# Kernel tuning notes

Measured on AMD Instinct MI355X. Metric: run time of the kernel, lower is better.

Reference implementation:

```python
import jax, jax.numpy as jnp
import numpy as np

# --- SLAYER hyperparameters (from netParams) ---
THETA = 10.0        # spike threshold
TAU_SR = 10.0       # SRM alpha-kernel time constant (ms)
TAU_RHO = 1.0       # surrogate-gradient width
SCALE_RHO = 1.0     # surrogate-gradient scale
TS = 1.0            # simulation step (ms)
T_SAMPLE = 300      # number of time steps
K_LEN = 64          # truncated SRM kernel length

N_BATCH, N_IN, N_HID, N_OUT = 128, 784, 410, 10


def srm_kernel():
    # SRM-alpha kernel eps(t) = (t/tau) * exp(1 - t/tau), sampled at Ts, eps(0)=0
    t = jnp.arange(K_LEN, dtype=jnp.float32) * TS
    return (t / TAU_SR) * jnp.exp(1.0 - t / TAU_SR)


def psp(x):
    # Causal FIR filtering along time: out[t] = sum_k eps[k] * x[t-k]
    # x: [N, C, T]
    n, c, t = x.shape
    kern = srm_kernel()
    lhs = x.reshape(n * c, 1, t)
    rhs = kern[::-1].reshape(1, 1, K_LEN)  # flip: conv_general_dilated is cross-correlation
    out = jax.lax.conv_general_dilated(
        lhs, rhs, window_strides=(1,), padding=[(K_LEN - 1, 0)],
        dimension_numbers=("NCH", "OIH", "NCH"))
    return out.reshape(n, c, t)


@jax.custom_vjp
def spike_fn(u):
    # Heaviside threshold with surrogate gradient rho(u) = (scale/tau) * exp(-|u-theta|/tau)
    return (u >= THETA).astype(u.dtype)

def _spike_fwd(u):
    return spike_fn(u), u

def _spike_bwd(u, g):
    return (g * (SCALE_RHO / TAU_RHO) * jnp.exp(-jnp.abs(u - THETA) / TAU_RHO),)

spike_fn.defvjp(_spike_fwd, _spike_bwd)


def setup_inputs() -> dict:
    key = jax.random.key(0)
    k1, k2, k3, k4 = jax.random.split(key, 4)
    img = jax.random.uniform(k1, (N_BATCH, N_IN), dtype=jnp.float32)
    rand_u = jax.random.uniform(k2, (N_BATCH, N_IN, T_SAMPLE), dtype=jnp.float32)
    W1 = jax.random.normal(k3, (N_HID, N_IN), dtype=jnp.float32)
    W2 = jax.random.normal(k4, (N_OUT, N_HID), dtype=jnp.float32)
    return {"img": img, "rand_u": rand_u, "W1": W1, "W2": W2}


def reference(img, rand_u, W1, W2):
    # Poisson spike encoding: spike whenever uniform noise < pixel intensity
    s0 = (rand_u < img[:, :, None]).astype(jnp.float32)        # [N, 784, T]
    # fc1 (dense over spatial features, shared over time) -> psp -> spike
    a1 = jnp.einsum("nit,oi->not", s0, W1)                     # [N, 410, T]
    s1 = spike_fn(psp(a1))
    # fc2 -> psp -> spike
    a2 = jnp.einsum("nht,oh->not", s1, W2)                     # [N, 10, T]
    s2 = spike_fn(psp(a2))
    return s2
```

## Files before the change

### kernel.cpp

```cpp
#include <hip/hip_runtime.h>
#include <cstdint>
#include <cstddef>

#define N_B 128
#define N_I 784
#define N_H 410
#define N_O 10
#define TT  300
#define KL  64
#define NK  832
#define NKS 13
#define NTILES 26
#define NDIG 4
#define NKS2 7
#define S1_TILE 4800
#define S1_NSTRIDE 134400
#define SEGL 19
#define SEGL2 10
#define NWG1 (NTILES * N_B)
#define WPX  (NWG1 / 8)
#define DBYTES (NTILES * NKS * 1024)

typedef int v4i __attribute__((ext_vector_type(4)));

__device__ __forceinline__ void glds16(const void* g, void* l) {
  __builtin_amdgcn_global_load_lds(
      (const __attribute__((address_space(1))) uint32_t*)g,
      (__attribute__((address_space(3))) uint32_t*)l, 16, 0, 0);
}

__global__ void k_pack(const float* __restrict__ rand_u, const float* __restrict__ img,
                       uint8_t* __restrict__ s0b) {
  int t = blockIdx.x * 64 + threadIdx.x;
  int w2 = blockIdx.y;
  int n = blockIdx.z;
  if (t >= TT) return;
  const float* rb = rand_u + (size_t)n * N_I * TT + t;
  const float* ib = img + (size_t)n * N_I;
  uint8_t* dst = s0b + ((size_t)n * TT + t) * NK + w2 * 64;
  int kb = w2 * 64;
  #pragma unroll
  for (int g = 0; g < 4; ++g) {
    uint32_t wd[4];
    #pragma unroll
    for (int q = 0; q < 4; ++q) {
      uint32_t v = 0;
      #pragma unroll
      for (int b = 0; b < 4; ++b) {
        int i = kb + g * 16 + q * 4 + b;
        float r = (i < N_I) ? rb[(size_t)i * TT] : 2.0f;
        float p = (i < N_I) ? ib[i] : 0.0f;
        v |= (r < p ? 1u : 0u) << (8 * b);
      }
      wd[q] = v;
    }
    v4i o; o[0] = (int)wd[0]; o[1] = (int)wd[1]; o[2] = (int)wd[2]; o[3] = (int)wd[3];
    *(v4i*)(dst + g * 16) = o;
  }
}

__global__ void k_bprepall(const float* __restrict__ W1, const float* __restrict__ W2,
                           v4i* __restrict__ Bf, v4i* __restrict__ Bf2) {
  int bid  = blockIdx.x;
  int lane = threadIdx.x;
  if (bid < NDIG * NTILES * NKS) {
    int ks   = bid % NKS;
    int rest = bid / NKS;
    int nt   = rest % NTILES;
    int d    = rest / NTILES;
    int o     = nt * 16 + (lane & 15);
    int kbase = ks * 64 + (lane >> 4) * 16;
    uint32_t wds[4] = {0, 0, 0, 0};
    for (int j = 0; j < 16; ++j) {
      int k = kbase + j;
      int dig = 0;
      if (o < N_H && k < N_I) {
        double w = (double)W1[(size_t)o * N_I + k];
        int r = (int)llround(w * 268435456.0);
        for (int dd = 0; dd <= d; ++dd) {
          dig = (int)(int8_t)(uint8_t)(r & 255);
          r = (r - dig) >> 8;
        }
      }
      wds[j >> 2] |= ((uint32_t)(uint8_t)(int8_t)dig) << (8 * (j & 3));
    }
    v4i v; v[0] = (int)wds[0]; v[1] = (int)wds[1]; v[2] = (int)wds[2]; v[3] = (int)wds[3];
    Bf[(size_t)bid * 64 + lane] = v;
  } else {
    int b2 = bid - NDIG * NTILES * NKS;
    int ks = b2 % NKS2, d = b2 / NKS2;
    int o     = lane & 15;
    int kbase = ks * 64 + (lane >> 4) * 16;
    uint32_t wds[4] = {0, 0, 0, 0};
    for (int j = 0; j < 16; ++j) {
      int k = kbase + j;
      int dig = 0;
      if (o < N_O && k < N_H) {
        double w = (double)W2[(size_t)o * N_H + k];
        int r = (int)llround(w * 268435456.0);
        for (int dd = 0; dd <= d; ++dd) {
          dig = (int)(int8_t)(uint8_t)(r & 255);
          r = (r - dig) >> 8;
        }
      }
      wds[j >> 2] |= ((uint32_t)(uint8_t)(int8_t)dig) << (8 * (j & 3));
    }
    v4i v; v[0] = (int)wds[0]; v[1] = (int)wds[1]; v[2] = (int)wds[2]; v[3] = (int)wds[3];
    Bf2[(size_t)b2 * 64 + lane] = v;
  }
}

__global__ __launch_bounds__(256) void k_fused2(const uint8_t* __restrict__ s0b,
                                                const v4i* __restrict__ Bf,
                                                uint8_t* __restrict__ s1) {
  __shared__ __align__(16) uint8_t smem[73728];
  uint8_t* bufA = smem;
  uint8_t* bufB = smem + 40960;
  double (*tile)[17] = (double (*)[17])smem;

  int tid = threadIdx.x;
  int wave = tid >> 6, lane = tid & 63;
  int bid = blockIdx.x;
  int sw = (bid & 7) * WPX + (bid >> 3);
  int n = sw / NTILES, nt = sw % NTILES;
  int lrow = lane & 15, quad = lane >> 4;

  const uint8_t* an0 = s0b + (size_t)n * TT * NK;
  int arow = wave * 80 + (lane >> 2);
  int acol = (lane & 3) * 16;
  const uint8_t* bfb = (const uint8_t*)Bf + (size_t)nt * NKS * 1024 + (size_t)lane * 16;

  auto STAGE = [&](int k, int par) {
    uint8_t* ad = bufA + par * 20480 + wave * 5120;
    #pragma unroll
    for (int c = 0; c < 5; ++c) {
      int r = arow + c * 16; if (r > TT - 1) r = TT - 1;
      glds16(an0 + (size_t)r * NK + (size_t)k * 64 + acol, ad + c * 1024);
    }
    uint8_t* bd = bufB + par * 16384 + wave * 4096;
    #pragma unroll
    for (int d = 0; d < NDIG; ++d)
      glds16(bfb + (size_t)d * DBYTES + (size_t)k * 1024, bd + d * 1024);
  };
  auto LDA = [&](int par, v4i* a) {
    const uint8_t* base = bufA + par * 20480 + wave * 5120 + quad * 16;
    #pragma unroll
    for (int m = 0; m < 5; ++m)
      a[m] = *(const v4i*)(base + (size_t)(m * 16 + lrow) * 64);
  };
  auto LDB = [&](int par, v4i* b) {
    const uint8_t* base = bufB + par * 16384 + wave * 4096 + lane * 16;
    #pragma unroll
    for (int d = 0; d < NDIG; ++d)
      b[d] = *(const v4i*)(base + (size_t)d * 1024);
  };

  v4i acc[5][NDIG];
  #pragma unroll
  for (int m = 0; m < 5; ++m)
    #pragma unroll
    for (int d = 0; d < NDIG; ++d) { acc[m][d][0]=0; acc[m][d][1]=0; acc[m][d][2]=0; acc[m][d][3]=0; }

  STAGE(0, 0);
  STAGE(1, 1);
  asm volatile("s_waitcnt vmcnt(9)" ::: "memory");
  v4i acur[5], bcur[NDIG], anxt[5], bnxt[NDIG];
  LDA(0, acur); LDB(0, bcur);
  asm volatile("s_waitcnt lgkmcnt(0)" ::: "memory");
  __builtin_amdgcn_sched_barrier(0);
  STAGE(2, 0);

  #pragma unroll
  for (int ks = 0; ks < NKS; ++ks) {
    if (ks < NKS - 2) { asm volatile("s_waitcnt vmcnt(9)" ::: "memory"); }
    else              { asm volatile("s_waitcnt vmcnt(0)" ::: "memory"); }
    int pn = (ks + 1) & 1;
    if (ks < NKS - 1) { LDA(pn, anxt); LDB(pn, bnxt); }
    #pragma unroll
    for (int m = 0; m < 5; ++m)
      #pragma unroll
      for (int d = 0; d < NDIG; ++d)
        acc[m][d] = __builtin_amdgcn_mfma_i32_16x16x64_i8(acur[m], bcur[d], acc[m][d], 0, 0, 0);
    asm volatile("s_waitcnt lgkmcnt(0)" ::: "memory");
    __builtin_amdgcn_sched_barrier(0);
    if (ks < NKS - 3) STAGE(ks + 3, (ks + 3) & 1);
    if (ks < NKS - 1) {
      #pragma unroll
      for (int m = 0; m < 5; ++m) acur[m] = anxt[m];
      #pragma unroll
      for (int d = 0; d < NDIG; ++d) bcur[d] = bnxt[d];
    }
  }

  __syncthreads();

  #pragma unroll
  for (int m5 = 0; m5 < 5; ++m5)
    #pragma unroll
    for (int r = 0; r < 4; ++r) {
      int m = wave * 80 + m5 * 16 + quad * 4 + r;
      if (m < TT) {
        double v = (double)acc[m5][0][r]
                 + 256.0      * (double)acc[m5][1][r]
                 + 65536.0    * (double)acc[m5][2][r]
                 + 16777216.0 * (double)acc[m5][3][r];
        tile[m][lrow] = v;
      }
    }
  __syncthreads();

  {
    int col = tid & 15;
    int seg = tid >> 4;
    int T0 = seg * SEGL;
    int Wc = T0 - 63; if (Wc < 0) Wc = 0;
    const double q   = exp(-0.1);
    const double q64 = exp(-6.4);
    const double cS  = (exp(1.0) / 10.0) * (1.0 / 268435456.0);
    double s1a = 0.0, s2a = 0.0, s1b = 0.0, s2b = 0.0;
    uint8_t* sb = s1 + (size_t)n * S1_NSTRIDE + (size_t)nt * S1_TILE + col;
    for (int j = 0; j < 63; ++j) {
      int t = T0 - 63 + j;
      int tc = (t < 0) ? 0 : t;
      double xa = (t >= 0) ? tile[tc][col] : 0.0;
      s2a = q * (s2a + s1a);
      s1a = q * s1a + xa;
    }
    for (int j = 0; j < SEGL; ++j) {
      int t = T0 + j;
      int tc = (t > TT - 1) ? TT - 1 : t;
      int tb = t - 64;
      int tbc = (tb < 0) ? 0 : tb;
      double xa = tile[tc][col];
      double xb = (tb >= Wc) ? tile[tbc][col] : 0.0;
      s2b = q * (s2b + s1b);
      s1b = q * s1b + xb;
      s2a = q * (s2a + s1a);
      s1a = q * s1a + xa;
      double y = cS * (s2a - q64 * (s2b + 64.0 * s1b));
      if (t < TT) sb[(size_t)t * 16] = (y >= 10.0) ? 1 : 0;
    }
  }
}

__global__ __launch_bounds__(256) void k_l2f(const uint8_t* __restrict__ s1,
                                             const v4i* __restrict__ Bf2,
                                             float* __restrict__ out) {
  __shared__ double tile2[TT][17];
  int tid = threadIdx.x;
  int wave = tid >> 6, lane = tid & 63;
  int half = blockIdx.x, n = blockIdx.y;
  int lrow = lane & 15, quad = lane >> 4;
  const uint8_t* s1n = s1 + (size_t)n * S1_NSTRIDE;
  for (int mt = wave; mt < 19; mt += 4) {
    int m0 = mt * 16;
    int trow = m0 + lrow; if (trow > TT - 1) trow = TT - 1;
    v4i acc[NDIG];
    #pragma unroll
    for (int d = 0; d < NDIG; ++d) { acc[d][0]=0; acc[d][1]=0; acc[d][2]=0; acc[d][3]=0; }
    for (int ks = 0; ks < NKS2; ++ks) {
      v4i af = *(const v4i*)(s1n + (size_t)(ks * 4 + quad) * S1_TILE + (size_t)trow * 16);
      #pragma unroll
      for (int d = 0; d < NDIG; ++d) {
        v4i bf = Bf2[(size_t)(d * NKS2 + ks) * 64 + lane];
        acc[d] = __builtin_amdgcn_mfma_i32_16x16x64_i8(af, bf, acc[d], 0, 0, 0);
      }
    }
    #pragma unroll
    for (int r = 0; r < 4; ++r) {
      int m = m0 + quad * 4 + r;
      if (m < TT && lrow < N_O) {
        double v = (double)acc[0][r]
                 + 256.0      * (double)acc[1][r]
                 + 65536.0    * (double)acc[2][r]
                 + 16777216.0 * (double)acc[3][r];
        tile2[m][lrow] = v;
      }
    }
  }
  __syncthreads();

  {
    int col = tid & 15;
    int seg = half * 16 + (tid >> 4);
    int T0 = seg * SEGL2;
    int Wc = T0 - 63; if (Wc < 0) Wc = 0;
    const double q   = exp(-0.1);
    const double q64 = exp(-6.4);
    const double cS  = (exp(1.0) / 10.0) * (1.0 / 268435456.0);
    double s1a = 0.0, s2a = 0.0, s1b = 0.0, s2b = 0.0;
    float* ob = out + (size_t)n * N_O * TT + (size_t)col * TT;
    for (int j = 0; j < 63; ++j) {
      int t = T0 - 63 + j;
      int tc = (t < 0) ? 0 : t;
      tc = (tc > TT - 1) ? TT - 1 : tc;
      double xa = (t >= 0 && t < TT) ? tile2[tc][col] : 0.0;
      s2a = q * (s2a + s1a);
      s1a = q * s1a + xa;
    }
    for (int j = 0; j < SEGL2; ++j) {
      int t = T0 + j;
      int tc = (t > TT - 1) ? TT - 1 : t;
      int tb = t - 64;
      int tbc = (tb < 0) ? 0 : tb;
      tbc = (tbc > TT - 1) ? TT - 1 : tbc;
      double xa = tile2[tc][col];
      double xb = (tb >= Wc) ? tile2[tbc][col] : 0.0;
      s2b = q * (s2b + s1b);
      s1b = q * s1b + xb;
      s2a = q * (s2a + s1a);
      s1a = q * s1a + xa;
      double y = cS * (s2a - q64 * (s2b + 64.0 * s1b));
      if (t < TT && col < N_O) ob[t] = (y >= 10.0) ? 1.0f : 0.0f;
    }
  }
}

extern "C" void kernel_launch(void* const* d_in, const int* in_sizes, int n_in,
                              void* d_out, int out_size, void* d_ws, size_t ws_size,
                              hipStream_t stream) {
  const float* img   = (const float*)d_in[0];
  const float* randu = (const float*)d_in[1];
  const float* W1    = (const float*)d_in[2];
  const float* W2    = (const float*)d_in[3];
  float* out = (float*)d_out;

  char* ws = (char*)d_ws;
  size_t off = 0;
  auto alloc = [&](size_t bytes) -> void* {
    void* p = ws + off;
    off = (off + bytes + 511) & ~(size_t)511;
    return p;
  };
  uint8_t*  s0b = (uint8_t*) alloc((size_t)N_B * TT * NK);
  v4i*      Bf  = (v4i*)     alloc((size_t)NDIG * NTILES * NKS * 64 * 16);
  v4i*      Bf2 = (v4i*)     alloc((size_t)NDIG * NKS2 * 64 * 16);
  uint8_t*  s1  = (uint8_t*) alloc((size_t)N_B * S1_NSTRIDE);
  if (off > ws_size) return;

  k_pack    <<<dim3(5, NKS, N_B), 64, 0, stream>>>(randu, img, s0b);
  k_bprepall<<<dim3(NDIG * NTILES * NKS + NDIG * NKS2), 64, 0, stream>>>(W1, W2, Bf, Bf2);
  k_fused2  <<<dim3(NWG1), 256, 0, stream>>>(s0b, Bf, s1);
  k_l2f     <<<dim3(2, N_B), 256, 0, stream>>>(s1, Bf2, out);
}
```

Before: 311.6 us.

## Merge prep kernels and restructure GEMM staging with shared B tiles and barriers

Merges the spike-packing and weight-prep kernels into one launch to cut one kernel launch. In the int8 GEMM, each wave now stages only one digit slice of B, and all waves share it through LDS. B uses triple buffering, so the LDS footprint drops from 72KB to 52KB, which may allow more workgroups per CU. The register-level prefetch of A/B fragments is replaced by per-step LDS reads after a workgroup barrier. This adds barrier synchronisation and removes the register double-buffering.

```diff
diff --git a/kernel.cpp b/kernel.cpp
--- a/kernel.cpp
+++ b/kernel.cpp
@@ -20,6 +20,8 @@
 #define NWG1 (NTILES * N_B)
 #define WPX  (NWG1 / 8)
 #define DBYTES (NTILES * NKS * 1024)
+#define PACKBLK (5 * NKS * N_B)
+#define PREPBLK (NDIG * NTILES * NKS + NDIG * NKS2)
 
 typedef int v4i __attribute__((ext_vector_type(4)));
 
@@ -29,40 +31,42 @@
       (__attribute__((address_space(3))) uint32_t*)l, 16, 0, 0);
 }
 
-__global__ void k_pack(const float* __restrict__ rand_u, const float* __restrict__ img,
-                       uint8_t* __restrict__ s0b) {
-  int t = blockIdx.x * 64 + threadIdx.x;
-  int w2 = blockIdx.y;
-  int n = blockIdx.z;
-  if (t >= TT) return;
-  const float* rb = rand_u + (size_t)n * N_I * TT + t;
-  const float* ib = img + (size_t)n * N_I;
-  uint8_t* dst = s0b + ((size_t)n * TT + t) * NK + w2 * 64;
-  int kb = w2 * 64;
-  #pragma unroll
-  for (int g = 0; g < 4; ++g) {
-    uint32_t wd[4];
-    #pragma unroll
-    for (int q = 0; q < 4; ++q) {
-      uint32_t v = 0;
-      #pragma unroll
-      for (int b = 0; b < 4; ++b) {
-        int i = kb + g * 16 + q * 4 + b;
-        float r = (i < N_I) ? rb[(size_t)i * TT] : 2.0f;
-        float p = (i < N_I) ? ib[i] : 0.0f;
-        v |= (r < p ? 1u : 0u) << (8 * b);
-      }
-      wd[q] = v;
-    }
-    v4i o; o[0] = (int)wd[0]; o[1] = (int)wd[1]; o[2] = (int)wd[2]; o[3] = (int)wd[3];
-    *(v4i*)(dst + g * 16) = o;
-  }
-}
-
-__global__ void k_bprepall(const float* __restrict__ W1, const float* __restrict__ W2,
-                           v4i* __restrict__ Bf, v4i* __restrict__ Bf2) {
-  int bid  = blockIdx.x;
+__global__ void k_prep(const float* __restrict__ rand_u, const float* __restrict__ img,
+                       const float* __restrict__ W1, const float* __restrict__ W2,
+                       uint8_t* __restrict__ s0b, v4i* __restrict__ Bf,
+                       v4i* __restrict__ Bf2) {
+  int bid0 = blockIdx.x;
   int lane = threadIdx.x;
+  if (bid0 < PACKBLK) {
+    int t  = (bid0 % 5) * 64 + lane;
+    int w2 = (bid0 / 5) % NKS;
+    int n  = bid0 / (5 * NKS);
+    if (t >= TT) return;
+    const float* rb = rand_u + (size_t)n * N_I * TT + t;
+    const float* ib = img + (size_t)n * N_I;
+    uint8_t* dst = s0b + ((size_t)n * TT + t) * NK + w2 * 64;
+    int kb = w2 * 64;
+    #pragma unroll
+    for (int g = 0; g < 4; ++g) {
+      uint32_t wd[4];
+      #pragma unroll
+      for (int q = 0; q < 4; ++q) {
+        uint32_t v = 0;
+        #pragma unroll
+        for (int b = 0; b < 4; ++b) {
+          int i = kb + g * 16 + q * 4 + b;
+          float r = (i < N_I) ? rb[(size_t)i * TT] : 2.0f;
+          float p = (i < N_I) ? ib[i] : 0.0f;
+          v |= (r < p ? 1u : 0u) << (8 * b);
+        }
+        wd[q] = v;
+      }
+      v4i o; o[0] = (int)wd[0]; o[1] = (int)wd[1]; o[2] = (int)wd[2]; o[3] = (int)wd[3];
+      *(v4i*)(dst + g * 16) = o;
+    }
+    return;
+  }
+  int bid = bid0 - PACKBLK;
   if (bid < NDIG * NTILES * NKS) {
     int ks   = bid % NKS;
     int rest = bid / NKS;
@@ -113,7 +117,7 @@
 __global__ __launch_bounds__(256) void k_fused2(const uint8_t* __restrict__ s0b,
                                                 const v4i* __restrict__ Bf,
                                                 uint8_t* __restrict__ s1) {
-  __shared__ __align__(16) uint8_t smem[73728];
+  __shared__ __align__(16) uint8_t smem[53248];
   uint8_t* bufA = smem;
   uint8_t* bufB = smem + 40960;
   double (*tile)[17] = (double (*)[17])smem;
@@ -126,33 +130,19 @@
   int lrow = lane & 15, quad = lane >> 4;
 
   const uint8_t* an0 = s0b + (size_t)n * TT * NK;
-  int arow = wave * 80 + (lane >> 2);
-  int acol = (lane & 3) * 16;
-  const uint8_t* bfb = (const uint8_t*)Bf + (size_t)nt * NKS * 1024 + (size_t)lane * 16;
-
-  auto STAGE = [&](int k, int par) {
-    uint8_t* ad = bufA + par * 20480 + wave * 5120;
+  int arow = wave * 80 + (lane & 15);
+  int acolg = (lane >> 4) * 16;
+  const uint8_t* bsrc = (const uint8_t*)Bf + (size_t)nt * NKS * 1024
+                      + (size_t)wave * DBYTES + (size_t)lane * 16;
+
+  auto STAGE = [&](int k, int pa, int pb) {
+    uint8_t* ad = bufA + pa * 20480 + wave * 5120;
     #pragma unroll
     for (int c = 0; c < 5; ++c) {
       int r = arow + c * 16; if (r > TT - 1) r = TT - 1;
-      glds16(an0 + (size_t)r * NK + (size_t)k * 64 + acol, ad + c * 1024);
-    }
-    uint8_t* bd = bufB + par * 16384 + wave * 4096;
-    #pragma unroll
-    for (int d = 0; d < NDIG; ++d)
-      glds16(bfb + (size_t)d * DBYTES + (size_t)k * 1024, bd + d * 1024);
-  };
-  auto LDA = [&](int par, v4i* a) {
-    const uint8_t* base = bufA + par * 20480 + wave * 5120 + quad * 16;
-    #pragma unroll
-    for (int m = 0; m < 5; ++m)
-      a[m] = *(const v4i*)(base + (size_t)(m * 16 + lrow) * 64);
-  };
-  auto LDB = [&](int par, v4i* b) {
-    const uint8_t* base = bufB + par * 16384 + wave * 4096 + lane * 16;
-    #pragma unroll
-    for (int d = 0; d < NDIG; ++d)
-      b[d] = *(const v4i*)(base + (size_t)d * 1024);
+      glds16(an0 + (size_t)r * NK + (size_t)k * 64 + acolg, ad + c * 1024);
+    }
+    glds16(bsrc + (size_t)k * 1024, bufB + pb * 4096 + wave * 1024);
   };
 
   v4i acc[5][NDIG];
@@ -161,35 +151,34 @@
     #pragma unroll
     for (int d = 0; d < NDIG; ++d) { acc[m][d][0]=0; acc[m][d][1]=0; acc[m][d][2]=0; acc[m][d][3]=0; }
 
-  STAGE(0, 0);
-  STAGE(1, 1);
-  asm volatile("s_waitcnt vmcnt(9)" ::: "memory");
-  v4i acur[5], bcur[NDIG], anxt[5], bnxt[NDIG];
-  LDA(0, acur); LDB(0, bcur);
-  asm volatile("s_waitcnt lgkmcnt(0)" ::: "memory");
-  __builtin_amdgcn_sched_barrier(0);
-  STAGE(2, 0);
+  STAGE(0, 0, 0);
+  STAGE(1, 1, 1);
 
   #pragma unroll
   for (int ks = 0; ks < NKS; ++ks) {
-    if (ks < NKS - 2) { asm volatile("s_waitcnt vmcnt(9)" ::: "memory"); }
+    if (ks < NKS - 1) { asm volatile("s_waitcnt vmcnt(6)" ::: "memory"); }
     else              { asm volatile("s_waitcnt vmcnt(0)" ::: "memory"); }
-    int pn = (ks + 1) & 1;
-    if (ks < NKS - 1) { LDA(pn, anxt); LDB(pn, bnxt); }
+    __builtin_amdgcn_s_barrier();
+    __builtin_amdgcn_sched_barrier(0);
+    v4i a[5], b[NDIG];
+    {
+      const uint8_t* base = bufA + (ks & 1) * 20480 + wave * 5120 + quad * 256 + lrow * 16;
+      #pragma unroll
+      for (int m = 0; m < 5; ++m) a[m] = *(const v4i*)(base + m * 1024);
+    }
+    {
+      const uint8_t* base = bufB + (ks % 3) * 4096 + lane * 16;
+      #pragma unroll
+      for (int d = 0; d < NDIG; ++d) b[d] = *(const v4i*)(base + d * 1024);
+    }
     #pragma unroll
     for (int m = 0; m < 5; ++m)
       #pragma unroll
       for (int d = 0; d < NDIG; ++d)
-        acc[m][d] = __builtin_amdgcn_mfma_i32_16x16x64_i8(acur[m], bcur[d], acc[m][d], 0, 0, 0);
+        acc[m][d] = __builtin_amdgcn_mfma_i32_16x16x64_i8(a[m], b[d], acc[m][d], 0, 0, 0);
     asm volatile("s_waitcnt lgkmcnt(0)" ::: "memory");
     __builtin_amdgcn_sched_barrier(0);
-    if (ks < NKS - 3) STAGE(ks + 3, (ks + 3) & 1);
-    if (ks < NKS - 1) {
-      #pragma unroll
-      for (int m = 0; m < 5; ++m) acur[m] = anxt[m];
-      #pragma unroll
-      for (int d = 0; d < NDIG; ++d) bcur[d] = bnxt[d];
-    }
+    if (ks <= NKS - 3) STAGE(ks + 2, (ks + 2) & 1, (ks + 2) % 3);
   }
 
   __syncthreads();
@@ -338,8 +327,7 @@
   uint8_t*  s1  = (uint8_t*) alloc((size_t)N_B * S1_NSTRIDE);
   if (off > ws_size) return;
 
-  k_pack    <<<dim3(5, NKS, N_B), 64, 0, stream>>>(randu, img, s0b);
-  k_bprepall<<<dim3(NDIG * NTILES * NKS + NDIG * NKS2), 64, 0, stream>>>(W1, W2, Bf, Bf2);
-  k_fused2  <<<dim3(NWG1), 256, 0, stream>>>(s0b, Bf, s1);
-  k_l2f     <<<dim3(2, N_B), 256, 0, stream>>>(s1, Bf2, out);
-}
+  k_prep  <<<dim3(PACKBLK + PREPBLK), 64, 0, stream>>>(randu, img, W1, W2, s0b, Bf, Bf2);
+  k_fused2<<<dim3(NWG1), 256, 0, stream>>>(s0b, Bf, s1);
+  k_l2f   <<<dim3(2, N_B), 256, 0, stream>>>(s1, Bf2, out);
+}
```

New measurement: 318.8 us. +2.3%, slower.
